# Optimization experiments

Hardware: AMD Instinct MI355X
Metric: run time of the kernel (lower is better)

Reference implementation:

```python
import jax, jax.numpy as jnp
import numpy as np

N_NODES = 50000
N_EDGES = 800000
D_IN = 256
D_OUT = 256
HEADS = (4, 4)
NEG_SLOPE = 0.2


def gat_conv(x, W, attn_l, attn_r, bias, src, dst, n_nodes, apply_elu):
    """DGL GATConv forward (no dropout, eval mode).
    x: [N, F_in], W: [F_in, H*D], attn_l/attn_r: [H, D], bias: [H*D].
    Returns [N, H, D].
    """
    H, D = attn_l.shape
    feat = (x @ W).reshape(n_nodes, H, D)                      # [N,H,D]
    el = jnp.einsum('nhd,hd->nh', feat, attn_l)                # [N,H]
    er = jnp.einsum('nhd,hd->nh', feat, attn_r)                # [N,H]
    e = jax.nn.leaky_relu(el[src] + er[dst], NEG_SLOPE)        # [E,H]
    # edge softmax over incoming edges of each dst node
    m = jax.ops.segment_max(e, dst, num_segments=n_nodes)      # [N,H]
    ex = jnp.exp(e - m[dst])                                   # [E,H]
    denom = jax.ops.segment_sum(ex, dst, num_segments=n_nodes) # [N,H]
    alpha = ex / denom[dst]                                    # [E,H]
    msg = feat[src] * alpha[..., None]                         # [E,H,D]
    out = jax.ops.segment_sum(msg, dst, num_segments=n_nodes)  # [N,H,D]
    out = out + bias.reshape(1, H, D)
    if apply_elu:
        out = jax.nn.elu(out)
    return out


def setup_inputs() -> dict:
    key = jax.random.key(0)
    ks = jax.random.split(key, 12)
    H1, H2 = HEADS
    D1 = D_OUT // H1
    D2 = D_OUT // H2
    x = jax.random.normal(ks[0], (N_NODES, D_IN), dtype=jnp.float32)
    src = jax.random.randint(ks[1], (N_EDGES,), 0, N_NODES, dtype=jnp.int32)
    dst = jax.random.randint(ks[2], (N_EDGES,), 0, N_NODES, dtype=jnp.int32)
    s1 = 1.0 / np.sqrt(D_IN)
    s2 = 1.0 / np.sqrt(D_OUT)
    W1 = jax.random.normal(ks[3], (D_IN, H1 * D1), dtype=jnp.float32) * s1
    al1 = jax.random.normal(ks[4], (H1, D1), dtype=jnp.float32) * s2
    ar1 = jax.random.normal(ks[5], (H1, D1), dtype=jnp.float32) * s2
    b1 = jnp.zeros((H1 * D1,), dtype=jnp.float32)
    W2 = jax.random.normal(ks[6], (D_OUT, H2 * D2), dtype=jnp.float32) * s2
    al2 = jax.random.normal(ks[7], (H2, D2), dtype=jnp.float32) * s2
    ar2 = jax.random.normal(ks[8], (H2, D2), dtype=jnp.float32) * s2
    b2 = jnp.zeros((H2 * D2,), dtype=jnp.float32)
    return {"x": x, "src": src, "dst": dst,
            "W1": W1, "al1": al1, "ar1": ar1, "b1": b1,
            "W2": W2, "al2": al2, "ar2": ar2, "b2": b2}


def reference(x, src, dst, W1, al1, ar1, b1, W2, al2, ar2, b2):
    h1 = gat_conv(x, W1, al1, ar1, b1, src, dst, N_NODES, apply_elu=True)
    h1 = h1.reshape(N_NODES, -1)                               # [N, 256]
    h2 = gat_conv(h1, W2, al2, ar2, b2, src, dst, N_NODES, apply_elu=False)
    h2 = h2.reshape(N_NODES, -1)                               # [N, 256]
    return jnp.concatenate([x, h1, h2], axis=1)                # [N, 768]
```

## Files before the change

kernel.cpp:

```cpp
#include <hip/hip_runtime.h>
#include <hip/hip_bf16.h>

#define N_NODES 50000
#define N_EDGES 800000
#define HEADS 4
#define FDIM 256
#define OUT_STRIDE 768
#define SCAN_B 256
#define NBLK ((N_NODES + SCAN_B - 1) / SCAN_B)

__device__ __forceinline__ float lrelu(float v) { return v > 0.f ? v : 0.2f * v; }

__global__ void k_copy_x(const float* __restrict__ x, float* __restrict__ out) {
    int idx = blockIdx.x * blockDim.x + threadIdx.x;
    if (idx >= N_NODES * 64) return;
    int n = idx >> 6, q = idx & 63;
    float4 v = *(const float4*)&x[(size_t)n * FDIM + q * 4];
    *(float4*)&out[(size_t)n * OUT_STRIDE + q * 4] = v;
}

#define BM 128
#define BN 128
#define BK 16
#define LDSP (BM + 4)
__global__ __launch_bounds__(256) void k_gemm(const float* __restrict__ A, int lda,
                                              const float* __restrict__ B,
                                              float* __restrict__ C, int M) {
    __shared__ float As[BK][LDSP];
    __shared__ float Bs[BK][LDSP];
    const int tid = threadIdx.x;
    const int tr = tid >> 4;
    const int tc = tid & 15;
    const int brow = blockIdx.x * BM;
    const int bcol = blockIdx.y * BN;
    float acc[2][2][4][4] = {};

    for (int k0 = 0; k0 < 256; k0 += BK) {
#pragma unroll
        for (int i = 0; i < 2; ++i) {
            int idx = tid + i * 256;
            int row = idx >> 2;
            int kq  = (idx & 3) * 4;
            int gr = brow + row;
            float4 v = make_float4(0.f, 0.f, 0.f, 0.f);
            if (gr < M) v = *(const float4*)&A[(size_t)gr * lda + k0 + kq];
            As[kq + 0][row] = v.x; As[kq + 1][row] = v.y;
            As[kq + 2][row] = v.z; As[kq + 3][row] = v.w;
        }
#pragma unroll
        for (int i = 0; i < 2; ++i) {
            int idx = tid + i * 256;
            int kk  = idx >> 5;
            int col = (idx & 31) * 4;
            *(float4*)&Bs[kk][col] = *(const float4*)&B[(size_t)(k0 + kk) * 256 + bcol + col];
        }
        __syncthreads();
#pragma unroll
        for (int kk = 0; kk < BK; ++kk) {
            float4 a0 = *(const float4*)&As[kk][tr * 4];
            float4 a1 = *(const float4*)&As[kk][64 + tr * 4];
            float4 b0 = *(const float4*)&Bs[kk][tc * 4];
            float4 b1 = *(const float4*)&Bs[kk][64 + tc * 4];
            const float av0[4] = {a0.x, a0.y, a0.z, a0.w};
            const float av1[4] = {a1.x, a1.y, a1.z, a1.w};
            const float bv0[4] = {b0.x, b0.y, b0.z, b0.w};
            const float bv1[4] = {b1.x, b1.y, b1.z, b1.w};
#pragma unroll
            for (int i = 0; i < 4; ++i)
#pragma unroll
                for (int j = 0; j < 4; ++j) {
                    acc[0][0][i][j] += av0[i] * bv0[j];
                    acc[0][1][i][j] += av0[i] * bv1[j];
                    acc[1][0][i][j] += av1[i] * bv0[j];
                    acc[1][1][i][j] += av1[i] * bv1[j];
                }
        }
        __syncthreads();
    }
#pragma unroll
    for (int bi = 0; bi < 2; ++bi)
#pragma unroll
        for (int i = 0; i < 4; ++i) {
            int gr = brow + bi * 64 + tr * 4 + i;
            if (gr >= M) continue;
#pragma unroll
            for (int bj = 0; bj < 2; ++bj) {
                float4 v = make_float4(acc[bi][bj][i][0], acc[bi][bj][i][1],
                                       acc[bi][bj][i][2], acc[bi][bj][i][3]);
                *(float4*)&C[(size_t)gr * 256 + bcol + bj * 64 + tc * 4] = v;
            }
        }
}

__global__ void k_el_er(const float* __restrict__ feat,
                        const float* __restrict__ al, const float* __restrict__ ar,
                        float* __restrict__ el, float* __restrict__ er) {
    int gtid = blockIdx.x * blockDim.x + threadIdx.x;
    int node = gtid >> 6;
    int lane = threadIdx.x & 63;
    if (node >= N_NODES) return;
    float4 f = *(const float4*)&feat[(size_t)node * FDIM + lane * 4];
    float4 a = *(const float4*)&al[lane * 4];
    float4 r = *(const float4*)&ar[lane * 4];
    float pl = f.x * a.x + f.y * a.y + f.z * a.z + f.w * a.w;
    float pr = f.x * r.x + f.y * r.y + f.z * r.z + f.w * r.w;
#pragma unroll
    for (int off = 8; off >= 1; off >>= 1) {
        pl += __shfl_xor(pl, off, 64);
        pr += __shfl_xor(pr, off, 64);
    }
    if ((lane & 15) == 0) {
        int h = lane >> 4;
        el[node * HEADS + h] = pl;
        er[node * HEADS + h] = pr;
    }
}

__global__ void k_zero_counts(int* __restrict__ counts) {
    int i = blockIdx.x * blockDim.x + threadIdx.x;
    if (i < N_NODES) counts[i] = 0;
}
__global__ void k_hist(const int* __restrict__ dst, int* __restrict__ counts) {
    int e = blockIdx.x * blockDim.x + threadIdx.x;
    if (e < N_EDGES) atomicAdd(&counts[dst[e]], 1);
}
__global__ void k_scan1(const int* __restrict__ counts, int* __restrict__ excl,
                        int* __restrict__ blocksums) {
    __shared__ int s[SCAN_B];
    int tid = threadIdx.x;
    int i = blockIdx.x * SCAN_B + tid;
    int v = (i < N_NODES) ? counts[i] : 0;
    s[tid] = v;
    __syncthreads();
    for (int off = 1; off < SCAN_B; off <<= 1) {
        int t = (tid >= off) ? s[tid - off] : 0;
        __syncthreads();
        s[tid] += t;
        __syncthreads();
    }
    if (i < N_NODES) excl[i] = s[tid] - v;
    if (tid == SCAN_B - 1) blocksums[blockIdx.x] = s[tid];
}
__global__ void k_scan2(int* __restrict__ blocksums) {
    __shared__ int s[SCAN_B];
    int tid = threadIdx.x;
    int v = (tid < NBLK) ? blocksums[tid] : 0;
    s[tid] = v;
    __syncthreads();
    for (int off = 1; off < SCAN_B; off <<= 1) {
        int t = (tid >= off) ? s[tid - off] : 0;
        __syncthreads();
        s[tid] += t;
        __syncthreads();
    }
    if (tid < NBLK) blocksums[tid] = s[tid] - v;
}
__global__ void k_scan3(const int* __restrict__ excl, const int* __restrict__ blocksums,
                        int* __restrict__ row_start, int* __restrict__ cursor) {
    int i = blockIdx.x * blockDim.x + threadIdx.x;
    if (i >= N_NODES) return;
    int r = excl[i] + blocksums[i >> 8];
    row_start[i] = r;
    cursor[i] = r;
}
__global__ void k_place(const int* __restrict__ src, const int* __restrict__ dst,
                        int* __restrict__ cursor, int* __restrict__ csr_src) {
    int e = blockIdx.x * blockDim.x + threadIdx.x;
    if (e >= N_EDGES) return;
    int pos = atomicAdd(&cursor[dst[e]], 1);
    csr_src[pos] = src[e];
}

__global__ void k_gather(const int* __restrict__ row_start, const int* __restrict__ counts,
                         const int* __restrict__ csr_src,
                         const float* __restrict__ feat,
                         const float* __restrict__ el, const float* __restrict__ er,
                         const float* __restrict__ bias,
                         float* __restrict__ out_slice, int apply_elu) {
    int gtid = blockIdx.x * blockDim.x + threadIdx.x;
    int node = gtid >> 6;
    if (node >= N_NODES) return;
    int lane = threadIdx.x & 63;
    int h = lane >> 4;
    float4 bv = *(const float4*)&bias[lane * 4];
    int start = row_start[node];
    int cnt = counts[node];
    float4 acc = make_float4(0.f, 0.f, 0.f, 0.f);
    if (cnt > 0) {
        float erd = er[node * HEADS + h];
        float m = -1e30f, denom = 0.f;
        for (int i = 0; i < cnt; ++i) {
            int s = csr_src[start + i];
            float v = lrelu(el[s * HEADS + h] + erd);
            float mn = fmaxf(m, v);
            float scale = __expf(m - mn);
            float ex = __expf(v - mn);
            m = mn;
            denom = denom * scale + ex;
            float4 f = *(const float4*)&feat[(size_t)s * FDIM + lane * 4];
            acc.x = acc.x * scale + ex * f.x;
            acc.y = acc.y * scale + ex * f.y;
            acc.z = acc.z * scale + ex * f.z;
            acc.w = acc.w * scale + ex * f.w;
        }
        float inv = 1.f / denom;
        acc.x = acc.x * inv + bv.x; acc.y = acc.y * inv + bv.y;
        acc.z = acc.z * inv + bv.z; acc.w = acc.w * inv + bv.w;
    } else {
        acc = bv;
    }
    if (apply_elu) {
        acc.x = acc.x > 0.f ? acc.x : expm1f(acc.x);
        acc.y = acc.y > 0.f ? acc.y : expm1f(acc.y);
        acc.z = acc.z > 0.f ? acc.z : expm1f(acc.z);
        acc.w = acc.w > 0.f ? acc.w : expm1f(acc.w);
    }
    *(float4*)&out_slice[(size_t)node * OUT_STRIDE + lane * 4] = acc;
}

static void run_layer(const float* in, int lda,
                      const float* W, const float* al, const float* ar, const float* bias,
                      float* out_slice, int apply_elu,
                      const int* row_start, const int* counts, const int* csr_src,
                      float* feat, float* el, float* er, hipStream_t stream) {
    dim3 ggrid((N_NODES + BM - 1) / BM, 256 / BN);
    k_gemm<<<ggrid, 256, 0, stream>>>(in, lda, W, feat, N_NODES);
    k_el_er<<<(N_NODES * 64 + 255) / 256, 256, 0, stream>>>(feat, al, ar, el, er);
    k_gather<<<(N_NODES * 64 + 255) / 256, 256, 0, stream>>>(
        row_start, counts, csr_src, feat, el, er, bias, out_slice, apply_elu);
}

extern "C" void kernel_launch(void* const* d_in, const int* in_sizes, int n_in,
                              void* d_out, int out_size, void* d_ws, size_t ws_size,
                              hipStream_t stream) {
    const float* x   = (const float*)d_in[0];
    const int*   src = (const int*)d_in[1];
    const int*   dst = (const int*)d_in[2];
    const float* W1  = (const float*)d_in[3];
    const float* al1 = (const float*)d_in[4];
    const float* ar1 = (const float*)d_in[5];
    const float* b1  = (const float*)d_in[6];
    const float* W2  = (const float*)d_in[7];
    const float* al2 = (const float*)d_in[8];
    const float* ar2 = (const float*)d_in[9];
    const float* b2  = (const float*)d_in[10];
    float* out = (float*)d_out;

    size_t need_bytes = ((size_t)N_NODES * FDIM + 2u * N_NODES * HEADS) * 4u
                      + ((size_t)4 * N_NODES + 256 + N_EDGES) * 4u;
    if (ws_size < need_bytes) return;

    float* ws        = (float*)d_ws;
    float* feat      = ws;
    float* el        = feat + (size_t)N_NODES * FDIM;
    float* er        = el + N_NODES * HEADS;
    int*   counts    = (int*)(er + N_NODES * HEADS);
    int*   excl      = counts + N_NODES;
    int*   row_start = excl + N_NODES;
    int*   cursor    = row_start + N_NODES;
    int*   blocksums = cursor + N_NODES;
    int*   csr_src   = blocksums + 256;

    k_zero_counts<<<(N_NODES + 255) / 256, 256, 0, stream>>>(counts);
    k_hist<<<(N_EDGES + 255) / 256, 256, 0, stream>>>(dst, counts);
    k_scan1<<<NBLK, SCAN_B, 0, stream>>>(counts, excl, blocksums);
    k_scan2<<<1, SCAN_B, 0, stream>>>(blocksums);
    k_scan3<<<(N_NODES + 255) / 256, 256, 0, stream>>>(excl, blocksums, row_start, cursor);
    k_place<<<(N_EDGES + 255) / 256, 256, 0, stream>>>(src, dst, cursor, csr_src);

    k_copy_x<<<(N_NODES * 64 + 255) / 256, 256, 0, stream>>>(x, out);

    run_layer(x, FDIM, W1, al1, ar1, b1, out + 256, 1,
              row_start, counts, csr_src, feat, el, er, stream);

    run_layer(out + 256, OUT_STRIDE, W2, al2, ar2, b2, out + 512, 0,
              row_start, counts, csr_src, feat, el, er, stream);
}
```

Baseline: 863.6 us.

## Fuse attention logit computation into GEMM epilogue with register-prefetched tiles

Folds the el/er attention dot products into the GEMM epilogue, using the accumulator registers and shuffle reductions across the 8 lanes that share a head. This removes the separate k_el_er kernel, which re-read the whole feature matrix, and saves one launch. The GEMM also changes to 64x128 tiles with BK=32, launch bounds (256,4), and register prefetching of the next k-tile so global loads overlap compute. The cost is higher register pressure and a different tile shape, which may reduce per-block reuse.

```diff
diff --git a/kernel.cpp b/kernel.cpp
--- a/kernel.cpp
+++ b/kernel.cpp
@@ -19,100 +19,142 @@
     *(float4*)&out[(size_t)n * OUT_STRIDE + q * 4] = v;
 }
 
-#define BM 128
+#define BM 64
 #define BN 128
-#define BK 16
-#define LDSP (BM + 4)
-__global__ __launch_bounds__(256) void k_gemm(const float* __restrict__ A, int lda,
-                                              const float* __restrict__ B,
-                                              float* __restrict__ C, int M) {
-    __shared__ float As[BK][LDSP];
-    __shared__ float Bs[BK][LDSP];
+#define BK 32
+#define LDA_S (BM + 4)
+#define LDB_S (BN + 4)
+__global__ __launch_bounds__(256, 4) void k_gemm(const float* __restrict__ A, int lda,
+                                                 const float* __restrict__ B,
+                                                 float* __restrict__ C, int M,
+                                                 const float* __restrict__ al,
+                                                 const float* __restrict__ ar,
+                                                 float* __restrict__ el,
+                                                 float* __restrict__ er) {
+    __shared__ float As[BK][LDA_S];
+    __shared__ float Bs[BK][LDB_S];
     const int tid = threadIdx.x;
     const int tr = tid >> 4;
     const int tc = tid & 15;
     const int brow = blockIdx.x * BM;
     const int bcol = blockIdx.y * BN;
-    float acc[2][2][4][4] = {};
+    float acc[4][8] = {};
+
+    float4 pa[2], pb[4];
+    int a_row[2];
+#pragma unroll
+    for (int i = 0; i < 2; ++i) {
+        int idx = tid + i * 256;
+        a_row[i] = idx >> 3;
+    }
+
+#pragma unroll
+    for (int i = 0; i < 2; ++i) {
+        int idx = tid + i * 256;
+        int gr = brow + a_row[i];
+        int kq = (idx & 7) * 4;
+        pa[i] = (gr < M) ? *(const float4*)&A[(size_t)gr * lda + kq]
+                         : make_float4(0.f, 0.f, 0.f, 0.f);
+    }
+#pragma unroll
+    for (int i = 0; i < 4; ++i) {
+        int idx = tid + i * 256;
+        int kk = idx >> 5;
+        int col = (idx & 31) * 4;
+        pb[i] = *(const float4*)&B[(size_t)kk * 256 + bcol + col];
+    }
 
     for (int k0 = 0; k0 < 256; k0 += BK) {
+        __syncthreads();
 #pragma unroll
         for (int i = 0; i < 2; ++i) {
             int idx = tid + i * 256;
-            int row = idx >> 2;
-            int kq  = (idx & 3) * 4;
-            int gr = brow + row;
-            float4 v = make_float4(0.f, 0.f, 0.f, 0.f);
-            if (gr < M) v = *(const float4*)&A[(size_t)gr * lda + k0 + kq];
-            As[kq + 0][row] = v.x; As[kq + 1][row] = v.y;
-            As[kq + 2][row] = v.z; As[kq + 3][row] = v.w;
-        }
-#pragma unroll
-        for (int i = 0; i < 2; ++i) {
+            int kq = (idx & 7) * 4;
+            As[kq + 0][a_row[i]] = pa[i].x;
+            As[kq + 1][a_row[i]] = pa[i].y;
+            As[kq + 2][a_row[i]] = pa[i].z;
+            As[kq + 3][a_row[i]] = pa[i].w;
+        }
+#pragma unroll
+        for (int i = 0; i < 4; ++i) {
             int idx = tid + i * 256;
-            int kk  = idx >> 5;
+            int kk = idx >> 5;
             int col = (idx & 31) * 4;
-            *(float4*)&Bs[kk][col] = *(const float4*)&B[(size_t)(k0 + kk) * 256 + bcol + col];
-        }
-        __syncthreads();
+            *(float4*)&Bs[kk][col] = pb[i];
+        }
+        __syncthreads();
+
+        int kn = k0 + BK;
+        if (kn < 256) {
+#pragma unroll
+            for (int i = 0; i < 2; ++i) {
+                int idx = tid + i * 256;
+                int gr = brow + a_row[i];
+                int kq = (idx & 7) * 4;
+                pa[i] = (gr < M) ? *(const float4*)&A[(size_t)gr * lda + kn + kq]
+                                 : make_float4(0.f, 0.f, 0.f, 0.f);
+            }
+#pragma unroll
+            for (int i = 0; i < 4; ++i) {
+                int idx = tid + i * 256;
+                int kk = idx >> 5;
+                int col = (idx & 31) * 4;
+                pb[i] = *(const float4*)&B[(size_t)(kn + kk) * 256 + bcol + col];
+            }
+        }
+
 #pragma unroll
         for (int kk = 0; kk < BK; ++kk) {
-            float4 a0 = *(const float4*)&As[kk][tr * 4];
-            float4 a1 = *(const float4*)&As[kk][64 + tr * 4];
-            float4 b0 = *(const float4*)&Bs[kk][tc * 4];
-            float4 b1 = *(const float4*)&Bs[kk][64 + tc * 4];
-            const float av0[4] = {a0.x, a0.y, a0.z, a0.w};
-            const float av1[4] = {a1.x, a1.y, a1.z, a1.w};
-            const float bv0[4] = {b0.x, b0.y, b0.z, b0.w};
-            const float bv1[4] = {b1.x, b1.y, b1.z, b1.w};
+            float4 a = *(const float4*)&As[kk][tr * 4];
+            float4 b0 = *(const float4*)&Bs[kk][tc * 8];
+            float4 b1 = *(const float4*)&Bs[kk][tc * 8 + 4];
+            const float av[4] = {a.x, a.y, a.z, a.w};
+            const float bv[8] = {b0.x, b0.y, b0.z, b0.w, b1.x, b1.y, b1.z, b1.w};
 #pragma unroll
             for (int i = 0; i < 4; ++i)
 #pragma unroll
-                for (int j = 0; j < 4; ++j) {
-                    acc[0][0][i][j] += av0[i] * bv0[j];
-                    acc[0][1][i][j] += av0[i] * bv1[j];
-                    acc[1][0][i][j] += av1[i] * bv0[j];
-                    acc[1][1][i][j] += av1[i] * bv1[j];
-                }
-        }
-        __syncthreads();
-    }
-#pragma unroll
-    for (int bi = 0; bi < 2; ++bi)
-#pragma unroll
-        for (int i = 0; i < 4; ++i) {
-            int gr = brow + bi * 64 + tr * 4 + i;
-            if (gr >= M) continue;
-#pragma unroll
-            for (int bj = 0; bj < 2; ++bj) {
-                float4 v = make_float4(acc[bi][bj][i][0], acc[bi][bj][i][1],
-                                       acc[bi][bj][i][2], acc[bi][bj][i][3]);
-                *(float4*)&C[(size_t)gr * 256 + bcol + bj * 64 + tc * 4] = v;
-            }
-        }
-}
-
-__global__ void k_el_er(const float* __restrict__ feat,
-                        const float* __restrict__ al, const float* __restrict__ ar,
-                        float* __restrict__ el, float* __restrict__ er) {
-    int gtid = blockIdx.x * blockDim.x + threadIdx.x;
-    int node = gtid >> 6;
-    int lane = threadIdx.x & 63;
-    if (node >= N_NODES) return;
-    float4 f = *(const float4*)&feat[(size_t)node * FDIM + lane * 4];
-    float4 a = *(const float4*)&al[lane * 4];
-    float4 r = *(const float4*)&ar[lane * 4];
-    float pl = f.x * a.x + f.y * a.y + f.z * a.z + f.w * a.w;
-    float pr = f.x * r.x + f.y * r.y + f.z * r.z + f.w * r.w;
-#pragma unroll
-    for (int off = 8; off >= 1; off >>= 1) {
-        pl += __shfl_xor(pl, off, 64);
-        pr += __shfl_xor(pr, off, 64);
-    }
-    if ((lane & 15) == 0) {
-        int h = lane >> 4;
-        el[node * HEADS + h] = pl;
-        er[node * HEADS + h] = pr;
+                for (int j = 0; j < 8; ++j)
+                    acc[i][j] += av[i] * bv[j];
+        }
+    }
+
+#pragma unroll
+    for (int i = 0; i < 4; ++i) {
+        int gr = brow + tr * 4 + i;
+        if (gr >= M) continue;
+        float4 v0 = make_float4(acc[i][0], acc[i][1], acc[i][2], acc[i][3]);
+        float4 v1 = make_float4(acc[i][4], acc[i][5], acc[i][6], acc[i][7]);
+        *(float4*)&C[(size_t)gr * 256 + bcol + tc * 8] = v0;
+        *(float4*)&C[(size_t)gr * 256 + bcol + tc * 8 + 4] = v1;
+    }
+
+    float alv[8], arv[8];
+    {
+        float4 a0 = *(const float4*)&al[bcol + tc * 8];
+        float4 a1 = *(const float4*)&al[bcol + tc * 8 + 4];
+        float4 r0 = *(const float4*)&ar[bcol + tc * 8];
+        float4 r1 = *(const float4*)&ar[bcol + tc * 8 + 4];
+        alv[0]=a0.x; alv[1]=a0.y; alv[2]=a0.z; alv[3]=a0.w;
+        alv[4]=a1.x; alv[5]=a1.y; alv[6]=a1.z; alv[7]=a1.w;
+        arv[0]=r0.x; arv[1]=r0.y; arv[2]=r0.z; arv[3]=r0.w;
+        arv[4]=r1.x; arv[5]=r1.y; arv[6]=r1.z; arv[7]=r1.w;
+    }
+    int h = (bcol >> 6) + (tc >> 3);
+#pragma unroll
+    for (int i = 0; i < 4; ++i) {
+        float pl = 0.f, pr = 0.f;
+#pragma unroll
+        for (int j = 0; j < 8; ++j) { pl += acc[i][j] * alv[j]; pr += acc[i][j] * arv[j]; }
+#pragma unroll
+        for (int off = 1; off <= 4; off <<= 1) {
+            pl += __shfl_xor(pl, off, 64);
+            pr += __shfl_xor(pr, off, 64);
+        }
+        int gr = brow + tr * 4 + i;
+        if ((tc & 7) == 0 && gr < M) {
+            el[gr * HEADS + h] = pl;
+            er[gr * HEADS + h] = pr;
+        }
     }
 }
 
@@ -224,8 +266,7 @@
                       const int* row_start, const int* counts, const int* csr_src,
                       float* feat, float* el, float* er, hipStream_t stream) {
     dim3 ggrid((N_NODES + BM - 1) / BM, 256 / BN);
-    k_gemm<<<ggrid, 256, 0, stream>>>(in, lda, W, feat, N_NODES);
-    k_el_er<<<(N_NODES * 64 + 255) / 256, 256, 0, stream>>>(feat, al, ar, el, er);
+    k_gemm<<<ggrid, 256, 0, stream>>>(in, lda, W, feat, N_NODES, al, ar, el, er);
     k_gather<<<(N_NODES * 64 + 255) / 256, 256, 0, stream>>>(
         row_start, counts, csr_src, feat, el, er, bias, out_slice, apply_elu);
 }
```

After: 844.4 us. -2.2%, faster.

## Replace FP32 GEMM with split-bf16 MFMA GEMM and fuse el/er projection

Applied to the files above, without the earlier changes.

Replaces the scalar FP32 tiled GEMM with a matrix-core kernel. Each operand is split into bf16 hi and lo parts, and three MFMA products (hi·hi, lo·hi, hi·lo) approximate FP32 accuracy. W is converted and transposed per layer by a small kernel. The A tile is stored in swizzled LDS. The per-head el/er attention dot products are computed in the GEMM epilogue, which removes a separate kernel and its re-read of feat. The cost is some precision loss and uncoalesced scalar stores of C.

```diff
diff --git a/kernel.cpp b/kernel.cpp
--- a/kernel.cpp
+++ b/kernel.cpp
@@ -9,7 +9,18 @@
 #define SCAN_B 256
 #define NBLK ((N_NODES + SCAN_B - 1) / SCAN_B)
 
+typedef __attribute__((ext_vector_type(8))) short short8;
+typedef __attribute__((ext_vector_type(4))) float f32x4;
+
 __device__ __forceinline__ float lrelu(float v) { return v > 0.f ? v : 0.2f * v; }
+
+__device__ __forceinline__ unsigned short f2bf(float f) {
+    unsigned u = __float_as_uint(f);
+    return (unsigned short)((u + 0x7fffu + ((u >> 16) & 1u)) >> 16);
+}
+__device__ __forceinline__ float bf2f(unsigned short s) {
+    return __uint_as_float(((unsigned)s) << 16);
+}
 
 __global__ void k_copy_x(const float* __restrict__ x, float* __restrict__ out) {
     int idx = blockIdx.x * blockDim.x + threadIdx.x;
@@ -19,100 +30,130 @@
     *(float4*)&out[(size_t)n * OUT_STRIDE + q * 4] = v;
 }
 
-#define BM 128
-#define BN 128
-#define BK 16
-#define LDSP (BM + 4)
-__global__ __launch_bounds__(256) void k_gemm(const float* __restrict__ A, int lda,
-                                              const float* __restrict__ B,
-                                              float* __restrict__ C, int M) {
-    __shared__ float As[BK][LDSP];
-    __shared__ float Bs[BK][LDSP];
+__global__ void k_convW(const float* __restrict__ W,
+                        unsigned short* __restrict__ bt_hi,
+                        unsigned short* __restrict__ bt_lo) {
+    int t = blockIdx.x * blockDim.x + threadIdx.x;
+    int k = t >> 8, col = t & 255;
+    float f = W[k * 256 + col];
+    unsigned short h = f2bf(f);
+    bt_hi[(size_t)col * 256 + k] = h;
+    bt_lo[(size_t)col * 256 + k] = f2bf(f - bf2f(h));
+}
+
+__device__ __forceinline__ int a_idx(int row, int cq) {
+    return row * 256 + ((cq ^ (row & 31)) << 3);
+}
+
+__global__ __launch_bounds__(512) void k_gemm_mfma(
+        const float* __restrict__ A, int lda,
+        const unsigned short* __restrict__ bt_hi, const unsigned short* __restrict__ bt_lo,
+        float* __restrict__ C, int M,
+        const float* __restrict__ al, const float* __restrict__ ar,
+        float* __restrict__ el, float* __restrict__ er) {
+    __shared__ __align__(16) unsigned short As_hi[64 * 256];
+    __shared__ __align__(16) unsigned short As_lo[64 * 256];
     const int tid = threadIdx.x;
-    const int tr = tid >> 4;
-    const int tc = tid & 15;
-    const int brow = blockIdx.x * BM;
-    const int bcol = blockIdx.y * BN;
-    float acc[2][2][4][4] = {};
-
-    for (int k0 = 0; k0 < 256; k0 += BK) {
-#pragma unroll
-        for (int i = 0; i < 2; ++i) {
-            int idx = tid + i * 256;
-            int row = idx >> 2;
-            int kq  = (idx & 3) * 4;
-            int gr = brow + row;
-            float4 v = make_float4(0.f, 0.f, 0.f, 0.f);
-            if (gr < M) v = *(const float4*)&A[(size_t)gr * lda + k0 + kq];
-            As[kq + 0][row] = v.x; As[kq + 1][row] = v.y;
-            As[kq + 2][row] = v.z; As[kq + 3][row] = v.w;
-        }
-#pragma unroll
-        for (int i = 0; i < 2; ++i) {
-            int idx = tid + i * 256;
-            int kk  = idx >> 5;
-            int col = (idx & 31) * 4;
-            *(float4*)&Bs[kk][col] = *(const float4*)&B[(size_t)(k0 + kk) * 256 + bcol + col];
-        }
-        __syncthreads();
-#pragma unroll
-        for (int kk = 0; kk < BK; ++kk) {
-            float4 a0 = *(const float4*)&As[kk][tr * 4];
-            float4 a1 = *(const float4*)&As[kk][64 + tr * 4];
-            float4 b0 = *(const float4*)&Bs[kk][tc * 4];
-            float4 b1 = *(const float4*)&Bs[kk][64 + tc * 4];
-            const float av0[4] = {a0.x, a0.y, a0.z, a0.w};
-            const float av1[4] = {a1.x, a1.y, a1.z, a1.w};
-            const float bv0[4] = {b0.x, b0.y, b0.z, b0.w};
-            const float bv1[4] = {b1.x, b1.y, b1.z, b1.w};
-#pragma unroll
-            for (int i = 0; i < 4; ++i)
-#pragma unroll
-                for (int j = 0; j < 4; ++j) {
-                    acc[0][0][i][j] += av0[i] * bv0[j];
-                    acc[0][1][i][j] += av0[i] * bv1[j];
-                    acc[1][0][i][j] += av1[i] * bv0[j];
-                    acc[1][1][i][j] += av1[i] * bv1[j];
+    const int brow = blockIdx.x * 64;
+
+    {
+        const int row = tid >> 3;
+        const int seg = tid & 7;
+        const int grow = brow + row;
+        const bool valid = grow < M;
+        const float* ap = A + (size_t)grow * lda + seg * 32;
+#pragma unroll
+        for (int c = 0; c < 4; ++c) {
+            float fv[8];
+            if (valid) {
+                float4 f0 = *(const float4*)(ap + c * 8);
+                float4 f1 = *(const float4*)(ap + c * 8 + 4);
+                fv[0]=f0.x; fv[1]=f0.y; fv[2]=f0.z; fv[3]=f0.w;
+                fv[4]=f1.x; fv[5]=f1.y; fv[6]=f1.z; fv[7]=f1.w;
+            } else {
+#pragma unroll
+                for (int j = 0; j < 8; ++j) fv[j] = 0.f;
+            }
+            short8 vh, vl;
+#pragma unroll
+            for (int j = 0; j < 8; ++j) {
+                unsigned short h = f2bf(fv[j]);
+                vh[j] = (short)h;
+                vl[j] = (short)f2bf(fv[j] - bf2f(h));
+            }
+            int idx = a_idx(row, seg * 4 + c);
+            *(short8*)&As_hi[idx] = vh;
+            *(short8*)&As_lo[idx] = vl;
+        }
+    }
+    __syncthreads();
+
+    const int lane = tid & 63;
+    const int w = tid >> 6;
+    const int wr = w >> 2;
+    const int wc = w & 3;
+    const int ln15 = lane & 15;
+    const int kg = lane >> 4;
+    f32x4 acc[2][4] = {};
+
+#pragma unroll 2
+    for (int ks = 0; ks < 8; ++ks) {
+        short8 ah[2], am[2];
+#pragma unroll
+        for (int rf = 0; rf < 2; ++rf) {
+            int idx = a_idx(wr * 32 + rf * 16 + ln15, ks * 4 + kg);
+            ah[rf] = *(const short8*)&As_hi[idx];
+            am[rf] = *(const short8*)&As_lo[idx];
+        }
+#pragma unroll
+        for (int cf = 0; cf < 4; ++cf) {
+            size_t boff = (size_t)(wc * 64 + cf * 16 + ln15) * 256 + ks * 32 + kg * 8;
+            short8 bh = *(const short8*)&bt_hi[boff];
+            short8 bl = *(const short8*)&bt_lo[boff];
+#pragma unroll
+            for (int rf = 0; rf < 2; ++rf) {
+                acc[rf][cf] = __builtin_amdgcn_mfma_f32_16x16x32_bf16(ah[rf], bh, acc[rf][cf], 0, 0, 0);
+                acc[rf][cf] = __builtin_amdgcn_mfma_f32_16x16x32_bf16(am[rf], bh, acc[rf][cf], 0, 0, 0);
+                acc[rf][cf] = __builtin_amdgcn_mfma_f32_16x16x32_bf16(ah[rf], bl, acc[rf][cf], 0, 0, 0);
+            }
+        }
+    }
+
+#pragma unroll
+    for (int rf = 0; rf < 2; ++rf) {
+        float pel[4] = {0.f, 0.f, 0.f, 0.f};
+        float per[4] = {0.f, 0.f, 0.f, 0.f};
+#pragma unroll
+        for (int cf = 0; cf < 4; ++cf) {
+            int gcol = wc * 64 + cf * 16 + ln15;
+            float alv = al[gcol], arv = ar[gcol];
+#pragma unroll
+            for (int reg = 0; reg < 4; ++reg) {
+                float v = acc[rf][cf][reg];
+                int gr = brow + wr * 32 + rf * 16 + kg * 4 + reg;
+                if (gr < M) C[(size_t)gr * 256 + gcol] = v;
+                pel[reg] += v * alv;
+                per[reg] += v * arv;
+            }
+        }
+#pragma unroll
+        for (int reg = 0; reg < 4; ++reg) {
+#pragma unroll
+            for (int off = 1; off <= 8; off <<= 1) {
+                pel[reg] += __shfl_xor(pel[reg], off, 64);
+                per[reg] += __shfl_xor(per[reg], off, 64);
+            }
+        }
+        if (ln15 == 0) {
+#pragma unroll
+            for (int reg = 0; reg < 4; ++reg) {
+                int gr = brow + wr * 32 + rf * 16 + kg * 4 + reg;
+                if (gr < M) {
+                    el[gr * HEADS + wc] = pel[reg];
+                    er[gr * HEADS + wc] = per[reg];
                 }
-        }
-        __syncthreads();
-    }
-#pragma unroll
-    for (int bi = 0; bi < 2; ++bi)
-#pragma unroll
-        for (int i = 0; i < 4; ++i) {
-            int gr = brow + bi * 64 + tr * 4 + i;
-            if (gr >= M) continue;
-#pragma unroll
-            for (int bj = 0; bj < 2; ++bj) {
-                float4 v = make_float4(acc[bi][bj][i][0], acc[bi][bj][i][1],
-                                       acc[bi][bj][i][2], acc[bi][bj][i][3]);
-                *(float4*)&C[(size_t)gr * 256 + bcol + bj * 64 + tc * 4] = v;
-            }
-        }
-}
-
-__global__ void k_el_er(const float* __restrict__ feat,
-                        const float* __restrict__ al, const float* __restrict__ ar,
-                        float* __restrict__ el, float* __restrict__ er) {
-    int gtid = blockIdx.x * blockDim.x + threadIdx.x;
-    int node = gtid >> 6;
-    int lane = threadIdx.x & 63;
-    if (node >= N_NODES) return;
-    float4 f = *(const float4*)&feat[(size_t)node * FDIM + lane * 4];
-    float4 a = *(const float4*)&al[lane * 4];
-    float4 r = *(const float4*)&ar[lane * 4];
-    float pl = f.x * a.x + f.y * a.y + f.z * a.z + f.w * a.w;
-    float pr = f.x * r.x + f.y * r.y + f.z * r.z + f.w * r.w;
-#pragma unroll
-    for (int off = 8; off >= 1; off >>= 1) {
-        pl += __shfl_xor(pl, off, 64);
-        pr += __shfl_xor(pr, off, 64);
-    }
-    if ((lane & 15) == 0) {
-        int h = lane >> 4;
-        el[node * HEADS + h] = pl;
-        er[node * HEADS + h] = pr;
+            }
+        }
     }
 }
 
@@ -222,10 +263,11 @@
                       const float* W, const float* al, const float* ar, const float* bias,
                       float* out_slice, int apply_elu,
                       const int* row_start, const int* counts, const int* csr_src,
-                      float* feat, float* el, float* er, hipStream_t stream) {
-    dim3 ggrid((N_NODES + BM - 1) / BM, 256 / BN);
-    k_gemm<<<ggrid, 256, 0, stream>>>(in, lda, W, feat, N_NODES);
-    k_el_er<<<(N_NODES * 64 + 255) / 256, 256, 0, stream>>>(feat, al, ar, el, er);
+                      float* feat, float* el, float* er,
+                      unsigned short* bt_hi, unsigned short* bt_lo, hipStream_t stream) {
+    k_convW<<<256, 256, 0, stream>>>(W, bt_hi, bt_lo);
+    k_gemm_mfma<<<(N_NODES + 63) / 64, 512, 0, stream>>>(
+        in, lda, bt_hi, bt_lo, feat, N_NODES, al, ar, el, er);
     k_gather<<<(N_NODES * 64 + 255) / 256, 256, 0, stream>>>(
         row_start, counts, csr_src, feat, el, er, bias, out_slice, apply_elu);
 }
@@ -247,7 +289,8 @@
     float* out = (float*)d_out;
 
     size_t need_bytes = ((size_t)N_NODES * FDIM + 2u * N_NODES * HEADS) * 4u
-                      + ((size_t)4 * N_NODES + 256 + N_EDGES) * 4u;
+                      + ((size_t)4 * N_NODES + 256 + N_EDGES) * 4u
+                      + 2u * 65536u * 2u;
     if (ws_size < need_bytes) return;
 
     float* ws        = (float*)d_ws;
@@ -260,6 +303,8 @@
     int*   cursor    = row_start + N_NODES;
     int*   blocksums = cursor + N_NODES;
     int*   csr_src   = blocksums + 256;
+    unsigned short* bt_hi = (unsigned short*)(csr_src + N_EDGES);
+    unsigned short* bt_lo = bt_hi + 65536;
 
     k_zero_counts<<<(N_NODES + 255) / 256, 256, 0, stream>>>(counts);
     k_hist<<<(N_EDGES + 255) / 256, 256, 0, stream>>>(dst, counts);
@@ -271,8 +316,8 @@
     k_copy_x<<<(N_NODES * 64 + 255) / 256, 256, 0, stream>>>(x, out);
 
     run_layer(x, FDIM, W1, al1, ar1, b1, out + 256, 1,
-              row_start, counts, csr_src, feat, el, er, stream);
+              row_start, counts, csr_src, feat, el, er, bt_hi, bt_lo, stream);
 
     run_layer(out + 256, OUT_STRIDE, W2, al2, ar2, b2, out + 512, 0,
-              row_start, counts, csr_src, feat, el, er, stream);
-}
+              row_start, counts, csr_src, feat, el, er, bt_hi, bt_lo, stream);
+}
```

After: 712.0 us. 17.6% less time.
